# Performance work log

Hardware: AMD Instinct MI355X
Metric: run time of the kernel (lower is better)

## Reference

```python
import jax, jax.numpy as jnp
import numpy as np

B, C, H, W = 8, 512, 64, 64
NH, D = 8, 64            # num_heads, head_dim (C = NH*D)
WH, WW = 8, 8            # window size
EPS = 1e-5
SCALE = D ** -0.5


def _layernorm(x, g, b):
    mu = jnp.mean(x, axis=-1, keepdims=True)
    var = jnp.mean((x - mu) ** 2, axis=-1, keepdims=True)
    return (x - mu) * jax.lax.rsqrt(var + EPS) * g + b


def _rope_cache(n, d):
    pos = jnp.arange(n, dtype=jnp.float32)
    inv_freq = 1.0 / (10000.0 ** (jnp.arange(0, d, 2, dtype=jnp.float32) / d))
    sinusoid = pos[:, None] * inv_freq[None, :]          # (n, d//2)
    return jnp.stack([jnp.sin(sinusoid), jnp.cos(sinusoid)], axis=-1).reshape(n, d)


def _apply_rope(x, rope):
    # x: (B, nH, N, d); rope: (N, d) packed [sin, cos] interleaved
    b, nh, n, d = x.shape
    x_ = x.reshape(b, nh, n, d // 2, 2)
    r = rope.reshape(n, d // 2, 2)
    sin, cos = r[..., 0], r[..., 1]                      # (N, d//2)
    x0, x1 = x_[..., 0], x_[..., 1]
    xr0 = x0 * cos - x1 * sin
    xr1 = x0 * sin + x1 * cos
    return jnp.stack([xr0, xr1], axis=-1).reshape(b, nh, n, d)


def _relative_index(wh, ww):
    ch, cw = np.meshgrid(np.arange(wh), np.arange(ww), indexing='ij')
    flat = np.stack([ch.reshape(-1), cw.reshape(-1)])    # (2, Ws)
    rel = flat[:, :, None] - flat[:, None, :]            # (2, Ws, Ws)
    rel = rel.transpose(1, 2, 0).astype(np.int64)
    rel[..., 0] += wh - 1
    rel[..., 1] += ww - 1
    rel[..., 0] *= 2 * ww - 1
    return jnp.asarray(rel.sum(-1))                      # (Ws, Ws)


def setup_inputs() -> dict:
    key = jax.random.key(0)
    ks = jax.random.split(key, 12)
    s = 0.02
    table_size = (2 * WH - 1) * (2 * WW - 1)
    return {
        'q':  jax.random.normal(ks[0], (B, C, H, W), jnp.float32),
        'kv': jax.random.normal(ks[1], (B, C, H, W), jnp.float32),
        'g_q':  jnp.ones((C,), jnp.float32),  'b_q_ln':  jnp.zeros((C,), jnp.float32),
        'g_kv': jnp.ones((C,), jnp.float32),  'b_kv_ln': jnp.zeros((C,), jnp.float32),
        'Wq': jax.random.normal(ks[2], (C, C), jnp.float32) * s, 'bq': jnp.zeros((C,), jnp.float32),
        'Wk': jax.random.normal(ks[3], (C, C), jnp.float32) * s, 'bk': jnp.zeros((C,), jnp.float32),
        'Wv': jax.random.normal(ks[4], (C, C), jnp.float32) * s, 'bv': jnp.zeros((C,), jnp.float32),
        'Wo': jax.random.normal(ks[5], (C, C), jnp.float32) * s, 'bo': jnp.zeros((C,), jnp.float32),
        'bias_table': jax.random.normal(ks[6], (table_size, NH), jnp.float32) * s,
    }


def reference(q, kv, g_q, b_q_ln, g_kv, b_kv_ln, Wq, bq, Wk, bk, Wv, bv, Wo, bo, bias_table):
    N = H * W
    Hn, Wn = H // WH, W // WW
    nw = Hn * Wn
    Ws = WH * WW

    # flatten NCHW -> (B, N, C)
    q_seq = q.reshape(B, C, N).transpose(0, 2, 1)
    kv_seq = kv.reshape(B, C, N).transpose(0, 2, 1)
    q_seq = _layernorm(q_seq, g_q, b_q_ln)
    kv_seq = _layernorm(kv_seq, g_kv, b_kv_ln)

    Q = (q_seq @ Wq.T + bq).reshape(B, N, NH, D).transpose(0, 2, 1, 3)   # (B,nH,N,d)
    K = (kv_seq @ Wk.T + bk).reshape(B, N, NH, D).transpose(0, 2, 1, 3)
    V = (kv_seq @ Wv.T + bv).reshape(B, N, NH, D).transpose(0, 2, 1, 3)

    rope = _rope_cache(N, D)
    Q = _apply_rope(Q, rope)
    K = _apply_rope(K, rope)

    # window partition: (B,nH,H,W,d) -> (nH, B*nw, Ws, d); head-major to match torch cat order
    def part(x):
        x = x.reshape(B, NH, Hn, WH, Wn, WW, D)
        return x.transpose(1, 0, 2, 4, 3, 5, 6).reshape(NH, B * nw, Ws, D)

    Qw, Kw, Vw = part(Q), part(K), part(V)

    attn = jnp.einsum('hnqd,hnkd->hnqk', Qw, Kw) * SCALE                 # (nH, B*nw, Ws, Ws)
    rel_idx = _relative_index(WH, WW)
    bias = bias_table[rel_idx.reshape(-1)].reshape(Ws, Ws, NH).transpose(2, 0, 1)  # (nH, Ws, Ws)
    attn = attn + bias[:, None, :, :]
    attn = jax.nn.softmax(attn, axis=-1)
    out_w = jnp.einsum('hnqk,hnkd->hnqd', attn, Vw)                      # (nH, B*nw, Ws, d)

    # window reverse + head concat -> (B, N, C)
    out = out_w.reshape(NH, B, Hn, Wn, WH, WW, D)
    out = out.transpose(1, 2, 4, 3, 5, 0, 6).reshape(B, N, NH * D)

    out = out @ Wo.T + bo
    out = out + q_seq                                                    # residual w/ normed q (as in source)
    return out.transpose(0, 2, 1).reshape(B, C, H, W)
```

## Files before the change

### kernel.cpp

```cpp
#include <hip/hip_runtime.h>


typedef unsigned short u16;
typedef __bf16 bf16x8 __attribute__((ext_vector_type(8)));
typedef float f32x4 __attribute__((ext_vector_type(4)));
typedef u16 u16x8 __attribute__((ext_vector_type(8)));
typedef u16 u16x4 __attribute__((ext_vector_type(4)));

__device__ __forceinline__ u16 f2bf(float f) {
    __bf16 h = (__bf16)f;
    return __builtin_bit_cast(u16, h);
}
__device__ __forceinline__ float bf2f(u16 u) {
    return (float)__builtin_bit_cast(__bf16, u);
}
__device__ __forceinline__ f32x4 mfma16(bf16x8 a, bf16x8 b, f32x4 c) {
    return __builtin_amdgcn_mfma_f32_16x16x32_bf16(a, b, c, 0, 0, 0);
}
__device__ __forceinline__ void gl_lds16(const u16* g, u16* l) {
    __builtin_amdgcn_global_load_lds((const __attribute__((address_space(1))) void*)g,
                                     (__attribute__((address_space(3))) void*)l, 16, 0, 0);
}
__device__ __forceinline__ int swapb(int n) {
    return (n & 0xE07) | ((n & 0x1C0) >> 3) | ((n & 0x038) << 3);
}

__global__ __launch_bounds__(256) void prep_kernel(
    const float* __restrict__ q, const float* __restrict__ kv,
    const float* __restrict__ g_q, const float* __restrict__ b_q,
    const float* __restrict__ g_kv, const float* __restrict__ b_kv,
    const float* __restrict__ Wq, const float* __restrict__ Wk,
    const float* __restrict__ Wv, const float* __restrict__ Wo,
    const float* __restrict__ btab,
    u16* __restrict__ qn, u16* __restrict__ kvn,
    u16* __restrict__ wq, u16* __restrict__ wk,
    u16* __restrict__ wv, u16* __restrict__ wo,
    float* __restrict__ rope, float* __restrict__ biasf)
{
    __shared__ u16 sX[512 * 36];
    __shared__ float sS[1024];
    __shared__ float sQm[1024];
    __shared__ float sMu[32], sInv[32];

    const int bidx = blockIdx.x;
    const int tid = threadIdx.x;

    if (bidx >= 2048) {
        int idx = (bidx - 2048) * 256 + tid;
        {
            int w = idx >> 18, e = idx & 262143;
            const float* src = (w == 0) ? Wq : (w == 1) ? Wk : (w == 2) ? Wv : Wo;
            u16* dst = (w == 0) ? wq : (w == 1) ? wk : (w == 2) ? wv : wo;
            dst[e] = f2bf(src[e]);
        }
        if (idx < 131072) {
            int n = idx >> 5, j = idx & 31;
            float inv = powf(10000.0f, -(float)j / 32.0f);
            float a = (float)n * inv;
            float s, c;
            sincosf(a, &s, &c);
            rope[n * 64 + 2 * j] = s;
            rope[n * 64 + 2 * j + 1] = c;
        }
        if (idx < 32768) {
            int qq = idx & 63, pp = (idx >> 6) & 63, h = idx >> 12;
            int r1 = pp >> 3, c1 = pp & 7, r2 = qq >> 3, c2 = qq & 7;
            int ri = (r1 - r2 + 7) * 15 + (c1 - c2 + 7);
            biasf[idx] = btab[ri * 8 + h];
        }
        return;
    }

    const float* x  = (bidx < 1024) ? q : kv;
    const float* g  = (bidx < 1024) ? g_q : g_kv;
    const float* be = (bidx < 1024) ? b_q : b_kv;
    u16* out = (bidx < 1024) ? qn : kvn;
    const int bid = bidx & 1023;

    const int b = bid >> 7, grp = bid & 127;
    const int nbase = grp << 5;
    const int t4 = tid & 7;
    const int cg = tid >> 3;

    const float* xp = x + ((size_t)b << 21) + nbase + (t4 << 2);
    float sm[4] = {0.f, 0.f, 0.f, 0.f}, sq2[4] = {0.f, 0.f, 0.f, 0.f};
#pragma unroll 4
    for (int it = 0; it < 16; it++) {
        int c = (it << 5) + cg;
        f32x4 v = *(const f32x4*)&xp[(size_t)c << 12];
        u16x4 h;
#pragma unroll
        for (int r = 0; r < 4; r++) {
            sm[r] += v[r];
            sq2[r] += v[r] * v[r];
            h[r] = f2bf(v[r]);
        }
        *(u16x4*)&sX[c * 36 + (t4 << 2)] = h;
    }
#pragma unroll
    for (int r = 0; r < 4; r++) {
        sS[tid * 4 + r] = sm[r];
        sQm[tid * 4 + r] = sq2[r];
    }
    __syncthreads();
    if (tid < 32) {
        int t4v = tid >> 2, r = tid & 3;
        float a = 0.f, q2 = 0.f;
#pragma unroll
        for (int c2 = 0; c2 < 32; c2++) {
            int i2 = ((c2 << 3) + t4v) * 4 + r;
            a += sS[i2];
            q2 += sQm[i2];
        }
        float mu = a * (1.f / 512.f);
        float var = q2 * (1.f / 512.f) - mu * mu;
        sMu[tid] = mu;
        sInv[tid] = rsqrtf(var + 1e-5f);
    }
    __syncthreads();

    const int t = tid >> 3;
    const int cs = (tid & 7) << 3;
    float mu = sMu[t], inv = sInv[t];
    int p = swapb(nbase + t);
    size_t orow = ((size_t)((b << 12) + p)) * 512;
#pragma unroll
    for (int it = 0; it < 8; it++) {
        int c0 = cs + (it << 6);
        f32x4 g0 = *(const f32x4*)&g[c0];
        f32x4 g1 = *(const f32x4*)&g[c0 + 4];
        f32x4 e0 = *(const f32x4*)&be[c0];
        f32x4 e1 = *(const f32x4*)&be[c0 + 4];
        u16x8 o;
#pragma unroll
        for (int k = 0; k < 8; k++) {
            float v = bf2f(sX[(c0 + k) * 36 + t]);
            float gg = (k < 4) ? g0[k] : g1[k - 4];
            float bb = (k < 4) ? e0[k] : e1[k - 4];
            o[k] = f2bf((v - mu) * inv * gg + bb);
        }
        *(u16x8*)&out[orow + c0] = o;
    }
}

#define SB() __builtin_amdgcn_sched_barrier(0)
#define BARRIER() do { SB(); __builtin_amdgcn_s_barrier(); SB(); } while (0)
#define VM4() asm volatile("s_waitcnt vmcnt(4)" ::: "memory")
#define VM0() asm volatile("s_waitcnt vmcnt(0)" ::: "memory")
#define STAGE_A(base, kt, kk) do { \
        const u16* _g = aSt + (kt) * 64 + (kk) * 32; \
        gl_lds16(_g, &smem[(base) + (kk) * 8192 + wid * 512]); \
        gl_lds16(_g + 65536, &smem[(base) + (kk) * 8192 + 4096 + wid * 512]); \
    } while (0)
#define STAGE_B(base, kt, kk) do { \
        const u16* _g = bSt + (kt) * 64 + (kk) * 32; \
        gl_lds16(_g, &smem[(base) + (kk) * 8192 + wid * 512]); \
        gl_lds16(_g + 65536, &smem[(base) + (kk) * 8192 + 4096 + wid * 512]); \
    } while (0)
#define LDA(base, kk, mh) do { \
        Af[0] = *(const bf16x8*)&smem[(base) + (kk) * 8192 + (mh) * 2048 + 0 * 512 + aOff]; \
        Af[1] = *(const bf16x8*)&smem[(base) + (kk) * 8192 + (mh) * 2048 + 1 * 512 + aOff]; \
        Af[2] = *(const bf16x8*)&smem[(base) + (kk) * 8192 + (mh) * 2048 + 2 * 512 + aOff]; \
        Af[3] = *(const bf16x8*)&smem[(base) + (kk) * 8192 + (mh) * 2048 + 3 * 512 + aOff]; \
    } while (0)
#define LDB(base, kk) do { \
        Bf[0] = *(const bf16x8*)&smem[(base) + (kk) * 8192 + 0 * 512 + bOff]; \
        Bf[1] = *(const bf16x8*)&smem[(base) + (kk) * 8192 + 1 * 512 + bOff]; \
        Bf[2] = *(const bf16x8*)&smem[(base) + (kk) * 8192 + 2 * 512 + bOff]; \
        Bf[3] = *(const bf16x8*)&smem[(base) + (kk) * 8192 + 3 * 512 + bOff]; \
    } while (0)
#define MMA(mh) do { \
        __builtin_amdgcn_s_setprio(1); \
        _Pragma("unroll") \
        for (int fi = 0; fi < 4; ++fi) \
            _Pragma("unroll") \
            for (int j = 0; j < 4; ++j) \
                acc[(mh) * 4 + fi][j] = mfma16(Af[fi], Bf[j], acc[(mh) * 4 + fi][j]); \
        __builtin_amdgcn_s_setprio(0); \
    } while (0)

#define MAIN_LOOP_8PHASE() \
    STAGE_A(AX, 0, 0); \
    STAGE_B(BX, 0, 0); \
    STAGE_A(AX, 0, 1); \
    STAGE_B(BX, 0, 1); \
    VM4(); \
    BARRIER(); \
    _Pragma("unroll") \
    for (int it = 0; it < 4; ++it) { \
        const bool last = (it == 3); \
        bf16x8 Af[4], Bf[4]; \
        LDA(AX, 0, 0); LDB(BX, 0); STAGE_A(AY, 2 * it + 1, 0); \
        BARRIER(); MMA(0); BARRIER(); \
        LDA(AX, 0, 1); STAGE_B(BY, 2 * it + 1, 0); \
        BARRIER(); MMA(1); VM4(); BARRIER(); \
        LDA(AX, 1, 0); LDB(BX, 1); STAGE_A(AY, 2 * it + 1, 1); \
        BARRIER(); MMA(0); BARRIER(); \
        LDA(AX, 1, 1); STAGE_B(BY, 2 * it + 1, 1); \
        BARRIER(); MMA(1); VM4(); BARRIER(); \
        LDA(AY, 0, 0); LDB(BY, 0); if (!last) STAGE_A(AX, 2 * it + 2, 0); \
        BARRIER(); MMA(0); BARRIER(); \
        LDA(AY, 0, 1); if (!last) STAGE_B(BX, 2 * it + 2, 0); \
        BARRIER(); MMA(1); \
        if (!last) { VM4(); } else { VM0(); } \
        BARRIER(); \
        LDA(AY, 1, 0); LDB(BY, 1); if (!last) STAGE_A(AX, 2 * it + 2, 1); \
        BARRIER(); MMA(0); BARRIER(); \
        LDA(AY, 1, 1); if (!last) STAGE_B(BX, 2 * it + 2, 1); \
        BARRIER(); MMA(1); if (!last) VM4(); BARRIER(); \
    }

__global__ __launch_bounds__(512, 2) void gemm_qkv(
    const u16* __restrict__ qn, const u16* __restrict__ kvn,
    const u16* __restrict__ wq, const u16* __restrict__ wk, const u16* __restrict__ wv,
    const float* __restrict__ bq, const float* __restrict__ bk, const float* __restrict__ bv,
    const float* __restrict__ rope,
    u16* __restrict__ Qr, u16* __restrict__ Kr, u16* __restrict__ VT)
{
    __shared__ __align__(16) u16 smem[65536];

    const int bid = blockIdx.x;
    const int swz = (bid & 7) * 96 + (bid >> 3);
    const int kind = swz >> 8;
    const int rem = swz & 255;
    const int n0 = (rem >> 7) << 8;
    const int m0 = (rem & 127) << 8;

    const u16* Asrc = (kind == 0) ? qn : kvn;
    const u16* W = (kind == 0) ? wq : (kind == 1) ? wk : wv;
    const float* bias = (kind == 0) ? bq : (kind == 1) ? bk : bv;

    const int tid = threadIdx.x;
    const int lane = tid & 63, wid = tid >> 6;
    const int ln = lane & 15, lq = lane >> 4;
    const int wr = wid >> 2, wc = wid & 3;

    const int rr = tid >> 2;
    const int cc = (tid & 3) ^ ((tid >> 3) & 3);
    const u16* aSt = Asrc + (size_t)(m0 + rr) * 512 + cc * 8;
    const u16* bSt = W + (size_t)(n0 + rr) * 512 + cc * 8;

    const int AX = 0, BX = 16384, AY = 32768, BY = 49152;
    const int swzc = lq ^ ((ln >> 1) & 3);
    const int aOff = wr * 4096 + ln * 32 + swzc * 8;
    const int bOff = wc * 2048 + ln * 32 + swzc * 8;

    f32x4 acc[8][4] = {};

    MAIN_LOOP_8PHASE();

    float bj[4];
#pragma unroll
    for (int j = 0; j < 4; ++j) bj[j] = bias[n0 + wc * 64 + j * 16 + ln];

    u16* sU = smem;

    if (kind < 2) {
        u16* Out = (kind == 0) ? Qr : Kr;
#pragma unroll
        for (int g = 0; g < 4; ++g) {
            __syncthreads();
            if (wr == (g >> 1)) {
                const int i0 = (g & 1) * 4;
#pragma unroll
                for (int di = 0; di < 4; ++di)
#pragma unroll
                    for (int j = 0; j < 4; ++j)
#pragma unroll
                        for (int r = 0; r < 4; ++r)
                            sU[(di * 16 + lq * 4 + r) * 264 + wc * 64 + j * 16 + ln] =
                                f2bf(acc[i0 + di][j][r] + bj[j]);
            }
            __syncthreads();
#pragma unroll
            for (int it = 0; it < 4; ++it) {
                int idx = it * 512 + tid;
                int row = idx >> 5;
                int cseg = (idx & 31) << 3;
                u16x8 v = *(const u16x8*)&sU[row * 264 + cseg];
                int t = m0 + g * 64 + row;
                int n = swapb(t & 4095);
                float f[8];
#pragma unroll
                for (int k = 0; k < 8; k++) f[k] = bf2f(v[k]);
                {
                    int d0 = cseg & 63;
                    const float* rp = &rope[n * 64 + d0];
                    f32x4 r0 = *(const f32x4*)rp;
                    f32x4 r1 = *(const f32x4*)(rp + 4);
#pragma unroll
                    for (int pp = 0; pp < 4; pp++) {
                        float sn = (pp < 2) ? r0[2 * pp] : r1[2 * (pp - 2)];
                        float cs2 = (pp < 2) ? r0[2 * pp + 1] : r1[2 * (pp - 2) + 1];
                        float x0 = f[2 * pp], x1 = f[2 * pp + 1];
                        f[2 * pp] = x0 * cs2 - x1 * sn;
                        f[2 * pp + 1] = x0 * sn + x1 * cs2;
                    }
                }
                u16x8 o;
#pragma unroll
                for (int k = 0; k < 8; k++) o[k] = f2bf(f[k]);
                *(u16x8*)&Out[(size_t)t * 512 + n0 + cseg] = o;
            }
        }
    } else {
        const int wq0 = m0 & 4095;
        const int bb = m0 >> 12;
#pragma unroll
        for (int g = 0; g < 4; ++g) {
            __syncthreads();
            if (wc == g) {
#pragma unroll
                for (int i = 0; i < 8; ++i)
#pragma unroll
                    for (int j = 0; j < 4; ++j) {
                        u16x4 pk;
#pragma unroll
                        for (int r = 0; r < 4; ++r) pk[r] = f2bf(acc[i][j][r] + bj[j]);
                        *(u16x4*)&sU[(j * 16 + ln) * 264 + wr * 128 + i * 16 + lq * 4] = pk;
                    }
            }
            __syncthreads();
#pragma unroll
            for (int it = 0; it < 4; ++it) {
                int idx = it * 512 + tid;
                int col = idx >> 5;
                int ch = (idx & 31) << 3;
                u16x8 v = *(const u16x8*)&sU[col * 264 + ch];
                int c = n0 + g * 64 + col;
                int hh = c >> 6, dd = c & 63;
                *(u16x8*)&VT[((size_t)((((bb << 3) + hh) << 6) + dd)) * 4096 + wq0 + ch] = v;
            }
        }
    }
}

__global__ __launch_bounds__(512, 2) void gemm_out(
    const u16* __restrict__ A, const u16* __restrict__ Bw,
    const float* __restrict__ bias, const u16* __restrict__ qn,
    float* __restrict__ Out)
{
    __shared__ __align__(16) u16 smem[65536];

    const int bid = blockIdx.x;
    const int swz = (bid & 7) * 32 + (bid >> 3);
    const int n0 = (swz >> 7) << 8;
    const int m0 = (swz & 127) << 8;

    const int tid = threadIdx.x;
    const int lane = tid & 63, wid = tid >> 6;
    const int ln = lane & 15, lq = lane >> 4;
    const int wr = wid >> 2, wc = wid & 3;

    const int rr = tid >> 2;
    const int cc = (tid & 3) ^ ((tid >> 3) & 3);
    const u16* aSt = A + (size_t)(m0 + rr) * 512 + cc * 8;
    const u16* bSt = Bw + (size_t)(n0 + rr) * 512 + cc * 8;

    const int AX = 0, BX = 16384, AY = 32768, BY = 49152;
    const int swzc = lq ^ ((ln >> 1) & 3);
    const int aOff = wr * 4096 + ln * 32 + swzc * 8;
    const int bOff = wc * 2048 + ln * 32 + swzc * 8;

    f32x4 acc[8][4] = {};

    MAIN_LOOP_8PHASE();

    float bj[4];
#pragma unroll
    for (int j = 0; j < 4; ++j) bj[j] = bias[n0 + wc * 64 + j * 16 + ln];

    u16* sR = smem;
#pragma unroll
    for (int g = 0; g < 4; ++g) {
        __syncthreads();
#pragma unroll
        for (int it = 0; it < 4; ++it) {
            int idx = it * 512 + tid;
            int row = idx >> 5, c8 = (idx & 31) << 3;
            *(u16x8*)&sR[row * 264 + c8] =
                *(const u16x8*)&qn[(size_t)(m0 + g * 64 + row) * 512 + n0 + c8];
        }
        __syncthreads();
        if (wr == (g >> 1)) {
            const int i0 = (g & 1) * 4;
#pragma unroll
            for (int di = 0; di < 4; ++di) {
                int t0 = m0 + g * 64 + di * 16 + lq * 4;
                int bb = t0 >> 12;
                int nb = swapb(t0 & 4095);
                int lr = di * 16 + lq * 4;
#pragma unroll
                for (int j = 0; j < 4; ++j) {
                    int c = wc * 64 + j * 16 + ln;
                    f32x4 v;
#pragma unroll
                    for (int r = 0; r < 4; ++r)
                        v[r] = acc[i0 + di][j][r] + bj[j] + bf2f(sR[(lr + r) * 264 + c]);
                    *(f32x4*)&Out[((size_t)((bb << 9) + n0 + c) << 12) + nb] = v;
                }
            }
        }
    }
}

#undef SB
#undef BARRIER
#undef VM4
#undef VM0
#undef STAGE_A
#undef STAGE_B
#undef LDA
#undef LDB
#undef MMA
#undef MAIN_LOOP_8PHASE

__global__ __launch_bounds__(256) void attn_kernel(
    const u16* __restrict__ Q, const u16* __restrict__ K, const u16* __restrict__ VT,
    const float* __restrict__ biasf, u16* __restrict__ Out)
{
    __shared__ u16 sQ[64 * 72];
    __shared__ u16 sK[64 * 72];
    __shared__ u16 sVT[64 * 72];
    __shared__ u16 sP[4][16 * 72];

    const int tid = threadIdx.x;
    const int h = blockIdx.x & 7;
    const int w = (blockIdx.x >> 3) & 63;
    const int b = blockIdx.x >> 9;
    const int lane = tid & 63, wave = tid >> 6;
    const int ln = lane & 15, lq = lane >> 4;

    const size_t qrow0 = (size_t)(b << 12) + w * 64;
    const size_t vrow0 = ((size_t)(((b << 3) + h) << 6)) * 4096 + w * 64;

#pragma unroll
    for (int ii = 0; ii < 2; ii++) {
        int idx = ii * 256 + tid;
        int row = idx >> 3, ch = (idx & 7) << 3;
        size_t ga = (qrow0 + row) * 512 + h * 64 + ch;
        *(u16x8*)&sQ[row * 72 + ch] = *(const u16x8*)&Q[ga];
        *(u16x8*)&sK[row * 72 + ch] = *(const u16x8*)&K[ga];
        *(u16x8*)&sVT[row * 72 + ch] = *(const u16x8*)&VT[vrow0 + (size_t)row * 4096 + ch];
    }
    __syncthreads();

    f32x4 s[4] = {};
#pragma unroll
    for (int ks = 0; ks < 2; ks++) {
        bf16x8 a = *(const bf16x8*)&sQ[(wave * 16 + ln) * 72 + ks * 32 + lq * 8];
#pragma unroll
        for (int j = 0; j < 4; j++) {
            bf16x8 bb = *(const bf16x8*)&sK[(j * 16 + ln) * 72 + ks * 32 + lq * 8];
            s[j] = mfma16(a, bb, s[j]);
        }
    }

    float sv[4][4];
#pragma unroll
    for (int r = 0; r < 4; r++) {
        const float* bp = &biasf[((h * 64 + wave * 16 + lq * 4 + r) << 6) + ln];
#pragma unroll
        for (int j = 0; j < 4; j++) sv[r][j] = s[j][r] * 0.125f + bp[j * 16];
    }
#pragma unroll
    for (int r = 0; r < 4; r++) {
        float m = fmaxf(fmaxf(sv[r][0], sv[r][1]), fmaxf(sv[r][2], sv[r][3]));
        m = fmaxf(m, __shfl_xor(m, 1));
        m = fmaxf(m, __shfl_xor(m, 2));
        m = fmaxf(m, __shfl_xor(m, 4));
        m = fmaxf(m, __shfl_xor(m, 8));
        float sum = 0.f;
#pragma unroll
        for (int j = 0; j < 4; j++) {
            sv[r][j] = __expf(sv[r][j] - m);
            sum += sv[r][j];
        }
        sum += __shfl_xor(sum, 1);
        sum += __shfl_xor(sum, 2);
        sum += __shfl_xor(sum, 4);
        sum += __shfl_xor(sum, 8);
        float rinv = 1.f / sum;
#pragma unroll
        for (int j = 0; j < 4; j++)
            sP[wave][(lq * 4 + r) * 72 + j * 16 + ln] = f2bf(sv[r][j] * rinv);
    }

    f32x4 o[4] = {};
#pragma unroll
    for (int ks = 0; ks < 2; ks++) {
        bf16x8 a = *(const bf16x8*)&sP[wave][ln * 72 + ks * 32 + lq * 8];
#pragma unroll
        for (int jd = 0; jd < 4; jd++) {
            bf16x8 bb = *(const bf16x8*)&sVT[(jd * 16 + ln) * 72 + ks * 32 + lq * 8];
            o[jd] = mfma16(a, bb, o[jd]);
        }
    }

#pragma unroll
    for (int r = 0; r < 4; r++)
#pragma unroll
        for (int jd = 0; jd < 4; jd++)
            sQ[(wave * 16 + lq * 4 + r) * 72 + jd * 16 + ln] = f2bf(o[jd][r]);
    __syncthreads();
#pragma unroll
    for (int ii = 0; ii < 2; ii++) {
        int idx = ii * 256 + tid;
        int row = idx >> 3, ch = (idx & 7) << 3;
        *(u16x8*)&Out[(qrow0 + row) * 512 + h * 64 + ch] = *(const u16x8*)&sQ[row * 72 + ch];
    }
}

extern "C" void kernel_launch(void* const* d_in, const int* in_sizes, int n_in,
                              void* d_out, int out_size, void* d_ws, size_t ws_size,
                              hipStream_t stream)
{
    const float* q    = (const float*)d_in[0];
    const float* kv   = (const float*)d_in[1];
    const float* g_q  = (const float*)d_in[2];
    const float* b_q  = (const float*)d_in[3];
    const float* g_kv = (const float*)d_in[4];
    const float* b_kv = (const float*)d_in[5];
    const float* Wq   = (const float*)d_in[6];
    const float* bq   = (const float*)d_in[7];
    const float* Wk   = (const float*)d_in[8];
    const float* bk   = (const float*)d_in[9];
    const float* Wv   = (const float*)d_in[10];
    const float* bv   = (const float*)d_in[11];
    const float* Wo   = (const float*)d_in[12];
    const float* bo   = (const float*)d_in[13];
    const float* btab = (const float*)d_in[14];

    char* ws = (char*)d_ws;
    u16* qn      = (u16*)(ws);
    u16* kvn     = (u16*)(ws + 33554432);
    u16* VT      = (u16*)(ws + 67108864);
    float* rope  = (float*)(ws + 100663296);
    float* biasf = (float*)(ws + 101711872);
    u16* wq      = (u16*)(ws + 101842944);
    u16* wk      = (u16*)(ws + 102367232);
    u16* wv      = (u16*)(ws + 102891520);
    u16* wo      = (u16*)(ws + 103415808);
    u16* aout    = kvn;
    u16* Qr      = (u16*)d_out;
    u16* Kr      = Qr + 16777216;

    prep_kernel<<<6144, 256, 0, stream>>>(q, kv, g_q, b_q, g_kv, b_kv,
                                          Wq, Wk, Wv, Wo, btab,
                                          qn, kvn, wq, wk, wv, wo, rope, biasf);
    gemm_qkv<<<768, 512, 0, stream>>>(qn, kvn, wq, wk, wv, bq, bk, bv, rope, Qr, Kr, VT);
    attn_kernel<<<4096, 256, 0, stream>>>(Qr, Kr, VT, biasf, aout);
    gemm_out<<<256, 512, 0, stream>>>(aout, wo, bo, qn, (float*)d_out);
}
```

Baseline: 344.2 us.

## Stage gemm_out epilogue through LDS for coalesced NCHW stores; two heads per attention block

Result: slower. 380.5 us (+10.5%).

```diff
diff --git a/kernel.cpp b/kernel.cpp
--- a/kernel.cpp
+++ b/kernel.cpp
@@ -370,36 +370,46 @@
 #pragma unroll
     for (int j = 0; j < 4; ++j) bj[j] = bias[n0 + wc * 64 + j * 16 + ln];
 
-    u16* sR = smem;
-#pragma unroll
-    for (int g = 0; g < 4; ++g) {
+    float* sOutF = (float*)smem;
+    u16* sRes = smem + 33280;
+    const int bb = m0 >> 12;
+    const int swb = swapb(m0 & 4095);
+    const size_t outBase = ((size_t)((bb << 9) + n0)) << 12;
+
+#pragma unroll
+    for (int cg = 0; cg < 4; ++cg) {
         __syncthreads();
 #pragma unroll
-        for (int it = 0; it < 4; ++it) {
-            int idx = it * 512 + tid;
-            int row = idx >> 5, c8 = (idx & 31) << 3;
-            *(u16x8*)&sR[row * 264 + c8] =
-                *(const u16x8*)&qn[(size_t)(m0 + g * 64 + row) * 512 + n0 + c8];
+        for (int itq = 0; itq < 4; ++itq) {
+            int idx = itq * 512 + tid;
+            int row = idx >> 3, c8 = (idx & 7) << 3;
+            *(u16x8*)&sRes[row * 72 + c8] =
+                *(const u16x8*)&qn[(size_t)(m0 + row) * 512 + n0 + cg * 64 + c8];
         }
         __syncthreads();
-        if (wr == (g >> 1)) {
-            const int i0 = (g & 1) * 4;
-#pragma unroll
-            for (int di = 0; di < 4; ++di) {
-                int t0 = m0 + g * 64 + di * 16 + lq * 4;
-                int bb = t0 >> 12;
-                int nb = swapb(t0 & 4095);
-                int lr = di * 16 + lq * 4;
-#pragma unroll
-                for (int j = 0; j < 4; ++j) {
-                    int c = wc * 64 + j * 16 + ln;
-                    f32x4 v;
-#pragma unroll
-                    for (int r = 0; r < 4; ++r)
-                        v[r] = acc[i0 + di][j][r] + bj[j] + bf2f(sR[(lr + r) * 264 + c]);
-                    *(f32x4*)&Out[((size_t)((bb << 9) + n0 + c) << 12) + nb] = v;
-                }
-            }
+        if (wc == cg) {
+#pragma unroll
+            for (int i = 0; i < 8; ++i)
+#pragma unroll
+                for (int j = 0; j < 4; ++j)
+#pragma unroll
+                    for (int r = 0; r < 4; ++r) {
+                        int row = wr * 128 + i * 16 + lq * 4 + r;
+                        int c = j * 16 + ln;
+                        sOutF[row * 65 + c] =
+                            acc[i][j][r] + bj[j] + bf2f(sRes[row * 72 + c]);
+                    }
+        }
+        __syncthreads();
+#pragma unroll
+        for (int li = 0; li < 8; ++li) {
+            int u = li * 512 + tid;
+            int c = u >> 6, r3 = (u >> 3) & 7, op = u & 7;
+            int base_i = ((op & 1) << 2) + (r3 << 3) + ((op >> 1) << 6);
+            f32x4 v;
+#pragma unroll
+            for (int r = 0; r < 4; ++r) v[r] = sOutF[(base_i + r) * 65 + c];
+            *(f32x4*)&Out[outBase + ((size_t)(cg * 64 + c) << 12) + swb + r3 * 64 + op * 4] = v;
         }
     }
 }
@@ -415,43 +425,18 @@
 #undef MMA
 #undef MAIN_LOOP_8PHASE
 
-__global__ __launch_bounds__(256) void attn_kernel(
-    const u16* __restrict__ Q, const u16* __restrict__ K, const u16* __restrict__ VT,
-    const float* __restrict__ biasf, u16* __restrict__ Out)
+__device__ __forceinline__ void attn_tile(
+    const u16* __restrict__ sQp, const u16* __restrict__ sKp,
+    const u16* __restrict__ sVTp, u16* __restrict__ sPp,
+    const float* __restrict__ biasf, int h, int wave, int ln, int lq, f32x4 o[4])
 {
-    __shared__ u16 sQ[64 * 72];
-    __shared__ u16 sK[64 * 72];
-    __shared__ u16 sVT[64 * 72];
-    __shared__ u16 sP[4][16 * 72];
-
-    const int tid = threadIdx.x;
-    const int h = blockIdx.x & 7;
-    const int w = (blockIdx.x >> 3) & 63;
-    const int b = blockIdx.x >> 9;
-    const int lane = tid & 63, wave = tid >> 6;
-    const int ln = lane & 15, lq = lane >> 4;
-
-    const size_t qrow0 = (size_t)(b << 12) + w * 64;
-    const size_t vrow0 = ((size_t)(((b << 3) + h) << 6)) * 4096 + w * 64;
-
-#pragma unroll
-    for (int ii = 0; ii < 2; ii++) {
-        int idx = ii * 256 + tid;
-        int row = idx >> 3, ch = (idx & 7) << 3;
-        size_t ga = (qrow0 + row) * 512 + h * 64 + ch;
-        *(u16x8*)&sQ[row * 72 + ch] = *(const u16x8*)&Q[ga];
-        *(u16x8*)&sK[row * 72 + ch] = *(const u16x8*)&K[ga];
-        *(u16x8*)&sVT[row * 72 + ch] = *(const u16x8*)&VT[vrow0 + (size_t)row * 4096 + ch];
-    }
-    __syncthreads();
-
     f32x4 s[4] = {};
 #pragma unroll
     for (int ks = 0; ks < 2; ks++) {
-        bf16x8 a = *(const bf16x8*)&sQ[(wave * 16 + ln) * 72 + ks * 32 + lq * 8];
+        bf16x8 a = *(const bf16x8*)&sQp[(wave * 16 + ln) * 72 + ks * 32 + lq * 8];
 #pragma unroll
         for (int j = 0; j < 4; j++) {
-            bf16x8 bb = *(const bf16x8*)&sK[(j * 16 + ln) * 72 + ks * 32 + lq * 8];
+            bf16x8 bb = *(const bf16x8*)&sKp[(j * 16 + ln) * 72 + ks * 32 + lq * 8];
             s[j] = mfma16(a, bb, s[j]);
         }
     }
@@ -483,31 +468,105 @@
         float rinv = 1.f / sum;
 #pragma unroll
         for (int j = 0; j < 4; j++)
-            sP[wave][(lq * 4 + r) * 72 + j * 16 + ln] = f2bf(sv[r][j] * rinv);
-    }
-
-    f32x4 o[4] = {};
+            sPp[(lq * 4 + r) * 72 + j * 16 + ln] = f2bf(sv[r][j] * rinv);
+    }
+
+    o[0] = f32x4{0.f, 0.f, 0.f, 0.f};
+    o[1] = f32x4{0.f, 0.f, 0.f, 0.f};
+    o[2] = f32x4{0.f, 0.f, 0.f, 0.f};
+    o[3] = f32x4{0.f, 0.f, 0.f, 0.f};
 #pragma unroll
     for (int ks = 0; ks < 2; ks++) {
-        bf16x8 a = *(const bf16x8*)&sP[wave][ln * 72 + ks * 32 + lq * 8];
+        bf16x8 a = *(const bf16x8*)&sPp[ln * 72 + ks * 32 + lq * 8];
 #pragma unroll
         for (int jd = 0; jd < 4; jd++) {
-            bf16x8 bb = *(const bf16x8*)&sVT[(jd * 16 + ln) * 72 + ks * 32 + lq * 8];
+            bf16x8 bb = *(const bf16x8*)&sVTp[(jd * 16 + ln) * 72 + ks * 32 + lq * 8];
             o[jd] = mfma16(a, bb, o[jd]);
         }
     }
-
-#pragma unroll
-    for (int r = 0; r < 4; r++)
-#pragma unroll
-        for (int jd = 0; jd < 4; jd++)
-            sQ[(wave * 16 + lq * 4 + r) * 72 + jd * 16 + ln] = f2bf(o[jd][r]);
-    __syncthreads();
+}
+
+__global__ __launch_bounds__(256) void attn_kernel(
+    const u16* __restrict__ Q, const u16* __restrict__ K, const u16* __restrict__ VT,
+    const float* __restrict__ biasf, u16* __restrict__ Out)
+{
+    __shared__ u16 sQ[2][64 * 72];
+    __shared__ u16 sK[2][64 * 72];
+    __shared__ u16 sVT[2][64 * 72];
+    __shared__ u16 sP[2][4][16 * 72];
+
+    const int tid = threadIdx.x;
+    const int code0 = blockIdx.x << 1;
+    const int h0 = code0 & 7;
+    const int w = (code0 >> 3) & 63;
+    const int b = code0 >> 9;
+    const int lane = tid & 63, wave = tid >> 6;
+    const int ln = lane & 15, lq = lane >> 4;
+
+    const size_t qrow0 = (size_t)(b << 12) + w * 64;
+
+    u16x8 rq[2][2], rk[2][2], rv[2][2];
+#pragma unroll
+    for (int t = 0; t < 2; ++t) {
+        const int h = h0 + t;
+        const size_t vrow0 = ((size_t)(((b << 3) + h) << 6)) * 4096 + w * 64;
+#pragma unroll
+        for (int ii = 0; ii < 2; ii++) {
+            int idx = ii * 256 + tid;
+            int rw = idx >> 3, ch = (idx & 7) << 3;
+            size_t ga = (qrow0 + rw) * 512 + h * 64 + ch;
+            rq[t][ii] = *(const u16x8*)&Q[ga];
+            rk[t][ii] = *(const u16x8*)&K[ga];
+            rv[t][ii] = *(const u16x8*)&VT[vrow0 + (size_t)rw * 4096 + ch];
+        }
+    }
 #pragma unroll
     for (int ii = 0; ii < 2; ii++) {
         int idx = ii * 256 + tid;
-        int row = idx >> 3, ch = (idx & 7) << 3;
-        *(u16x8*)&Out[(qrow0 + row) * 512 + h * 64 + ch] = *(const u16x8*)&sQ[row * 72 + ch];
+        int rw = idx >> 3, ch = (idx & 7) << 3;
+        *(u16x8*)&sQ[0][rw * 72 + ch] = rq[0][ii];
+        *(u16x8*)&sK[0][rw * 72 + ch] = rk[0][ii];
+        *(u16x8*)&sVT[0][rw * 72 + ch] = rv[0][ii];
+    }
+    __syncthreads();
+
+    f32x4 o[4];
+    attn_tile(sQ[0], sK[0], sVT[0], sP[0][wave], biasf, h0, wave, ln, lq, o);
+
+#pragma unroll
+    for (int ii = 0; ii < 2; ii++) {
+        int idx = ii * 256 + tid;
+        int rw = idx >> 3, ch = (idx & 7) << 3;
+        *(u16x8*)&sQ[1][rw * 72 + ch] = rq[1][ii];
+        *(u16x8*)&sK[1][rw * 72 + ch] = rk[1][ii];
+        *(u16x8*)&sVT[1][rw * 72 + ch] = rv[1][ii];
+    }
+#pragma unroll
+    for (int r = 0; r < 4; r++)
+#pragma unroll
+        for (int jd = 0; jd < 4; jd++)
+            sQ[0][(wave * 16 + lq * 4 + r) * 72 + jd * 16 + ln] = f2bf(o[jd][r]);
+    __syncthreads();
+
+#pragma unroll
+    for (int ii = 0; ii < 2; ii++) {
+        int idx = ii * 256 + tid;
+        int rw = idx >> 3, ch = (idx & 7) << 3;
+        *(u16x8*)&Out[(qrow0 + rw) * 512 + h0 * 64 + ch] = *(const u16x8*)&sQ[0][rw * 72 + ch];
+    }
+    attn_tile(sQ[1], sK[1], sVT[1], sP[1][wave], biasf, h0 + 1, wave, ln, lq, o);
+#pragma unroll
+    for (int r = 0; r < 4; r++)
+#pragma unroll
+        for (int jd = 0; jd < 4; jd++)
+            sQ[1][(wave * 16 + lq * 4 + r) * 72 + jd * 16 + ln] = f2bf(o[jd][r]);
+    __syncthreads();
+#pragma unroll
+    for (int ii = 0; ii < 2; ii++) {
+        int idx = ii * 256 + tid;
+        int rw = idx >> 3, ch = (idx & 7) << 3;
+        *(u16x8*)&Out[(qrow0 + rw) * 512 + (h0 + 1) * 64 + ch] =
+            *(const u16x8*)&sQ[1][rw * 72 + ch];
     }
 }
 
@@ -549,6 +608,6 @@
                                           Wq, Wk, Wv, Wo, btab,
                                           qn, kvn, wq, wk, wv, wo, rope, biasf);
     gemm_qkv<<<768, 512, 0, stream>>>(qn, kvn, wq, wk, wv, bq, bk, bv, rope, Qr, Kr, VT);
-    attn_kernel<<<4096, 256, 0, stream>>>(Qr, Kr, VT, biasf, aout);
+    attn_kernel<<<2048, 256, 0, stream>>>(Qr, Kr, VT, biasf, aout);
     gemm_out<<<256, 512, 0, stream>>>(aout, wo, bo, qn, (float*)d_out);
 }
```

## Make QKV GEMM persistent with cross-tile prefetch and restructure output epilogues

Applied to the files above, without the earlier changes.

After: 344.6 us. About the same (+0.1%).

```diff
diff --git a/kernel.cpp b/kernel.cpp
--- a/kernel.cpp
+++ b/kernel.cpp
@@ -4,6 +4,7 @@
 typedef unsigned short u16;
 typedef __bf16 bf16x8 __attribute__((ext_vector_type(8)));
 typedef float f32x4 __attribute__((ext_vector_type(4)));
+typedef float f32x2 __attribute__((ext_vector_type(2)));
 typedef u16 u16x8 __attribute__((ext_vector_type(8)));
 typedef u16 u16x4 __attribute__((ext_vector_type(4)));
 
@@ -46,23 +47,29 @@
     const int tid = threadIdx.x;
 
     if (bidx >= 2048) {
-        int idx = (bidx - 2048) * 256 + tid;
-        {
-            int w = idx >> 18, e = idx & 262143;
+        if (bidx < 3072) {
+            int idx = (bidx - 2048) * 256 + tid;
+            int w = idx >> 16, qd = idx & 65535;
             const float* src = (w == 0) ? Wq : (w == 1) ? Wk : (w == 2) ? Wv : Wo;
             u16* dst = (w == 0) ? wq : (w == 1) ? wk : (w == 2) ? wv : wo;
-            dst[e] = f2bf(src[e]);
-        }
-        if (idx < 131072) {
+            f32x4 v = *(const f32x4*)&src[qd * 4];
+            u16x4 h;
+#pragma unroll
+            for (int r = 0; r < 4; r++) h[r] = f2bf(v[r]);
+            *(u16x4*)&dst[qd * 4] = h;
+        } else if (bidx < 3584) {
+            int idx = (bidx - 3072) * 256 + tid;
             int n = idx >> 5, j = idx & 31;
             float inv = powf(10000.0f, -(float)j / 32.0f);
             float a = (float)n * inv;
             float s, c;
             sincosf(a, &s, &c);
-            rope[n * 64 + 2 * j] = s;
-            rope[n * 64 + 2 * j + 1] = c;
-        }
-        if (idx < 32768) {
+            f32x2 sc;
+            sc[0] = s;
+            sc[1] = c;
+            *(f32x2*)&rope[n * 64 + 2 * j] = sc;
+        } else {
+            int idx = (bidx - 3584) * 256 + tid;
             int qq = idx & 63, pp = (idx >> 6) & 63, h = idx >> 12;
             int r1 = pp >> 3, c1 = pp & 7, r2 = qq >> 3, c2 = qq & 7;
             int ri = (r1 - r2 + 7) * 15 + (c1 - c2 + 7);
@@ -84,7 +91,7 @@
 
     const float* xp = x + ((size_t)b << 21) + nbase + (t4 << 2);
     float sm[4] = {0.f, 0.f, 0.f, 0.f}, sq2[4] = {0.f, 0.f, 0.f, 0.f};
-#pragma unroll 4
+#pragma unroll 8
     for (int it = 0; it < 16; it++) {
         int c = (it << 5) + cg;
         f32x4 v = *(const f32x4*)&xp[(size_t)c << 12];
@@ -147,15 +154,17 @@
 #define BARRIER() do { SB(); __builtin_amdgcn_s_barrier(); SB(); } while (0)
 #define VM4() asm volatile("s_waitcnt vmcnt(4)" ::: "memory")
 #define VM0() asm volatile("s_waitcnt vmcnt(0)" ::: "memory")
-#define STAGE_A(base, kt, kk) do { \
-        const u16* _g = aSt + (kt) * 64 + (kk) * 32; \
+#define VM20() asm volatile("s_waitcnt vmcnt(20)" ::: "memory")
+#define STAGE_P(ptr, base, kt, kk) do { \
+        const u16* _g = (ptr) + (kt) * 64 + (kk) * 32; \
         gl_lds16(_g, &smem[(base) + (kk) * 8192 + wid * 512]); \
         gl_lds16(_g + 65536, &smem[(base) + (kk) * 8192 + 4096 + wid * 512]); \
     } while (0)
-#define STAGE_B(base, kt, kk) do { \
-        const u16* _g = bSt + (kt) * 64 + (kk) * 32; \
-        gl_lds16(_g, &smem[(base) + (kk) * 8192 + wid * 512]); \
-        gl_lds16(_g + 65536, &smem[(base) + (kk) * 8192 + 4096 + wid * 512]); \
+#define PROLOGUE4(aP, bP) do { \
+        STAGE_P(aP, AX, 0, 0); \
+        STAGE_P(bP, BX, 0, 0); \
+        STAGE_P(aP, AX, 0, 1); \
+        STAGE_P(bP, BX, 0, 1); \
     } while (0)
 #define LDA(base, kk, mh) do { \
         Af[0] = *(const bf16x8*)&smem[(base) + (kk) * 8192 + (mh) * 2048 + 0 * 512 + aOff]; \
@@ -179,34 +188,32 @@
         __builtin_amdgcn_s_setprio(0); \
     } while (0)
 
-#define MAIN_LOOP_8PHASE() \
-    STAGE_A(AX, 0, 0); \
-    STAGE_B(BX, 0, 0); \
-    STAGE_A(AX, 0, 1); \
-    STAGE_B(BX, 0, 1); \
-    VM4(); \
+#define MAIN_LOOP_8PHASE(WARM) \
+    if (WARM) { VM20(); } else { VM4(); } \
     BARRIER(); \
     _Pragma("unroll") \
     for (int it = 0; it < 4; ++it) { \
         const bool last = (it == 3); \
         bf16x8 Af[4], Bf[4]; \
-        LDA(AX, 0, 0); LDB(BX, 0); STAGE_A(AY, 2 * it + 1, 0); \
+        LDA(AX, 0, 0); LDB(BX, 0); STAGE_P(aSt, AY, 2 * it + 1, 0); \
         BARRIER(); MMA(0); BARRIER(); \
-        LDA(AX, 0, 1); STAGE_B(BY, 2 * it + 1, 0); \
+        LDA(AX, 0, 1); STAGE_P(bSt, BY, 2 * it + 1, 0); \
+        BARRIER(); MMA(1); \
+        if ((WARM) && it == 0) { VM20(); } else { VM4(); } \
+        BARRIER(); \
+        LDA(AX, 1, 0); LDB(BX, 1); STAGE_P(aSt, AY, 2 * it + 1, 1); \
+        BARRIER(); MMA(0); BARRIER(); \
+        LDA(AX, 1, 1); STAGE_P(bSt, BY, 2 * it + 1, 1); \
         BARRIER(); MMA(1); VM4(); BARRIER(); \
-        LDA(AX, 1, 0); LDB(BX, 1); STAGE_A(AY, 2 * it + 1, 1); \
+        LDA(AY, 0, 0); LDB(BY, 0); if (!last) STAGE_P(aSt, AX, 2 * it + 2, 0); \
         BARRIER(); MMA(0); BARRIER(); \
-        LDA(AX, 1, 1); STAGE_B(BY, 2 * it + 1, 1); \
-        BARRIER(); MMA(1); VM4(); BARRIER(); \
-        LDA(AY, 0, 0); LDB(BY, 0); if (!last) STAGE_A(AX, 2 * it + 2, 0); \
-        BARRIER(); MMA(0); BARRIER(); \
-        LDA(AY, 0, 1); if (!last) STAGE_B(BX, 2 * it + 2, 0); \
+        LDA(AY, 0, 1); if (!last) STAGE_P(bSt, BX, 2 * it + 2, 0); \
         BARRIER(); MMA(1); \
         if (!last) { VM4(); } else { VM0(); } \
         BARRIER(); \
-        LDA(AY, 1, 0); LDB(BY, 1); if (!last) STAGE_A(AX, 2 * it + 2, 1); \
+        LDA(AY, 1, 0); LDB(BY, 1); if (!last) STAGE_P(aSt, AX, 2 * it + 2, 1); \
         BARRIER(); MMA(0); BARRIER(); \
-        LDA(AY, 1, 1); if (!last) STAGE_B(BX, 2 * it + 2, 1); \
+        LDA(AY, 1, 1); if (!last) STAGE_P(bSt, BX, 2 * it + 2, 1); \
         BARRIER(); MMA(1); if (!last) VM4(); BARRIER(); \
     }
 
@@ -219,17 +226,7 @@
 {
     __shared__ __align__(16) u16 smem[65536];
 
-    const int bid = blockIdx.x;
-    const int swz = (bid & 7) * 96 + (bid >> 3);
-    const int kind = swz >> 8;
-    const int rem = swz & 255;
-    const int n0 = (rem >> 7) << 8;
-    const int m0 = (rem & 127) << 8;
-
-    const u16* Asrc = (kind == 0) ? qn : kvn;
-    const u16* W = (kind == 0) ? wq : (kind == 1) ? wk : wv;
-    const float* bias = (kind == 0) ? bq : (kind == 1) ? bk : bv;
-
+    const int p = blockIdx.x;
     const int tid = threadIdx.x;
     const int lane = tid & 63, wid = tid >> 6;
     const int ln = lane & 15, lq = lane >> 4;
@@ -237,102 +234,138 @@
 
     const int rr = tid >> 2;
     const int cc = (tid & 3) ^ ((tid >> 3) & 3);
-    const u16* aSt = Asrc + (size_t)(m0 + rr) * 512 + cc * 8;
-    const u16* bSt = W + (size_t)(n0 + rr) * 512 + cc * 8;
 
     const int AX = 0, BX = 16384, AY = 32768, BY = 49152;
     const int swzc = lq ^ ((ln >> 1) & 3);
     const int aOff = wr * 4096 + ln * 32 + swzc * 8;
     const int bOff = wc * 2048 + ln * 32 + swzc * 8;
 
-    f32x4 acc[8][4] = {};
-
-    MAIN_LOOP_8PHASE();
-
-    float bj[4];
-#pragma unroll
-    for (int j = 0; j < 4; ++j) bj[j] = bias[n0 + wc * 64 + j * 16 + ln];
-
-    u16* sU = smem;
-
-    if (kind < 2) {
-        u16* Out = (kind == 0) ? Qr : Kr;
-#pragma unroll
-        for (int g = 0; g < 4; ++g) {
-            __syncthreads();
-            if (wr == (g >> 1)) {
-                const int i0 = (g & 1) * 4;
-#pragma unroll
-                for (int di = 0; di < 4; ++di)
-#pragma unroll
-                    for (int j = 0; j < 4; ++j)
-#pragma unroll
-                        for (int r = 0; r < 4; ++r)
-                            sU[(di * 16 + lq * 4 + r) * 264 + wc * 64 + j * 16 + ln] =
-                                f2bf(acc[i0 + di][j][r] + bj[j]);
+    const u16* aSt;
+    const u16* bSt;
+    const float* bias;
+    int kind, n0, m0;
+
+#define DECODE(VID) do { \
+        int _swz = ((VID) & 7) * 96 + ((VID) >> 3); \
+        kind = _swz >> 8; \
+        int _rem = _swz & 255; \
+        n0 = (_rem >> 7) << 8; \
+        m0 = (_rem & 127) << 8; \
+        const u16* _As = (kind == 0) ? qn : kvn; \
+        const u16* _W = (kind == 0) ? wq : (kind == 1) ? wk : wv; \
+        bias = (kind == 0) ? bq : (kind == 1) ? bk : bv; \
+        aSt = _As + (size_t)(m0 + rr) * 512 + cc * 8; \
+        bSt = _W + (size_t)(n0 + rr) * 512 + cc * 8; \
+    } while (0)
+
+    f32x4 acc[8][4];
+
+    DECODE(p);
+    PROLOGUE4(aSt, bSt);
+
+#pragma unroll 1
+    for (int item = 0; item < 3; ++item) {
+#pragma unroll
+        for (int i = 0; i < 8; ++i)
+#pragma unroll
+            for (int j = 0; j < 4; ++j) acc[i][j] = f32x4{0.f, 0.f, 0.f, 0.f};
+
+        const bool warm = (item != 0);
+        MAIN_LOOP_8PHASE(warm);
+
+        const int ek = kind, en0 = n0, em0 = m0;
+        const float* ebias = bias;
+        if (item < 2) {
+            DECODE((item + 1) * 256 + p);
+            PROLOGUE4(aSt, bSt);
+        }
+
+        float bj[4];
+#pragma unroll
+        for (int j = 0; j < 4; ++j) bj[j] = ebias[en0 + wc * 64 + j * 16 + ln];
+
+        u16* sU = smem + 32768;
+
+        if (ek < 2) {
+            u16* Out = (ek == 0) ? Qr : Kr;
+#pragma unroll
+            for (int g = 0; g < 4; ++g) {
+                __syncthreads();
+                if (wr == (g >> 1)) {
+                    const int i0 = (g & 1) * 4;
+#pragma unroll
+                    for (int di = 0; di < 4; ++di)
+#pragma unroll
+                        for (int j = 0; j < 4; ++j)
+#pragma unroll
+                            for (int r = 0; r < 4; ++r)
+                                sU[(di * 16 + lq * 4 + r) * 264 + wc * 64 + j * 16 + ln] =
+                                    f2bf(acc[i0 + di][j][r] + bj[j]);
+                }
+                __syncthreads();
+#pragma unroll
+                for (int it = 0; it < 4; ++it) {
+                    int idx = it * 512 + tid;
+                    int row = idx >> 5;
+                    int cseg = (idx & 31) << 3;
+                    u16x8 v = *(const u16x8*)&sU[row * 264 + cseg];
+                    int t = em0 + g * 64 + row;
+                    int n = swapb(t & 4095);
+                    float f[8];
+#pragma unroll
+                    for (int k = 0; k < 8; k++) f[k] = bf2f(v[k]);
+                    {
+                        int d0 = cseg & 63;
+                        const float* rp = &rope[n * 64 + d0];
+                        f32x4 r0 = *(const f32x4*)rp;
+                        f32x4 r1 = *(const f32x4*)(rp + 4);
+#pragma unroll
+                        for (int pp = 0; pp < 4; pp++) {
+                            float sn = (pp < 2) ? r0[2 * pp] : r1[2 * (pp - 2)];
+                            float cs2 = (pp < 2) ? r0[2 * pp + 1] : r1[2 * (pp - 2) + 1];
+                            float x0 = f[2 * pp], x1 = f[2 * pp + 1];
+                            f[2 * pp] = x0 * cs2 - x1 * sn;
+                            f[2 * pp + 1] = x0 * sn + x1 * cs2;
+                        }
+                    }
+                    u16x8 o;
+#pragma unroll
+                    for (int k = 0; k < 8; k++) o[k] = f2bf(f[k]);
+                    *(u16x8*)&Out[(size_t)t * 512 + en0 + cseg] = o;
+                }
             }
-            __syncthreads();
-#pragma unroll
-            for (int it = 0; it < 4; ++it) {
-                int idx = it * 512 + tid;
-                int row = idx >> 5;
-                int cseg = (idx & 31) << 3;
-                u16x8 v = *(const u16x8*)&sU[row * 264 + cseg];
-                int t = m0 + g * 64 + row;
-                int n = swapb(t & 4095);
-                float f[8];
-#pragma unroll
-                for (int k = 0; k < 8; k++) f[k] = bf2f(v[k]);
-                {
-                    int d0 = cseg & 63;
-                    const float* rp = &rope[n * 64 + d0];
-                    f32x4 r0 = *(const f32x4*)rp;
-                    f32x4 r1 = *(const f32x4*)(rp + 4);
-#pragma unroll
-                    for (int pp = 0; pp < 4; pp++) {
-                        float sn = (pp < 2) ? r0[2 * pp] : r1[2 * (pp - 2)];
-                        float cs2 = (pp < 2) ? r0[2 * pp + 1] : r1[2 * (pp - 2) + 1];
-                        float x0 = f[2 * pp], x1 = f[2 * pp + 1];
-                        f[2 * pp] = x0 * cs2 - x1 * sn;
-                        f[2 * pp + 1] = x0 * sn + x1 * cs2;
-                    }
+        } else {
+            const int wq0 = em0 & 4095;
+            const int bb = em0 >> 12;
+#pragma unroll
+            for (int g = 0; g < 4; ++g) {
+                __syncthreads();
+                if (wc == g) {
+#pragma unroll
+                    for (int i = 0; i < 8; ++i)
+#pragma unroll
+                        for (int j = 0; j < 4; ++j) {
+                            u16x4 pk;
+#pragma unroll
+                            for (int r = 0; r < 4; ++r) pk[r] = f2bf(acc[i][j][r] + bj[j]);
+                            *(u16x4*)&sU[(j * 16 + ln) * 264 + wr * 128 + i * 16 + lq * 4] = pk;
+                        }
                 }
-                u16x8 o;
-#pragma unroll
-                for (int k = 0; k < 8; k++) o[k] = f2bf(f[k]);
-                *(u16x8*)&Out[(size_t)t * 512 + n0 + cseg] = o;
+                __syncthreads();
+#pragma unroll
+                for (int it = 0; it < 4; ++it) {
+                    int idx = it * 512 + tid;
+                    int col = idx >> 5;
+                    int ch = (idx & 31) << 3;
+                    u16x8 v = *(const u16x8*)&sU[col * 264 + ch];
+                    int c = en0 + g * 64 + col;
+                    int hh = c >> 6, dd = c & 63;
+                    *(u16x8*)&VT[((size_t)((((bb << 3) + hh) << 6) + dd)) * 4096 + wq0 + ch] = v;
+                }
             }
         }
-    } else {
-        const int wq0 = m0 & 4095;
-        const int bb = m0 >> 12;
-#pragma unroll
-        for (int g = 0; g < 4; ++g) {
-            __syncthreads();
-            if (wc == g) {
-#pragma unroll
-                for (int i = 0; i < 8; ++i)
-#pragma unroll
-                    for (int j = 0; j < 4; ++j) {
-                        u16x4 pk;
-#pragma unroll
-                        for (int r = 0; r < 4; ++r) pk[r] = f2bf(acc[i][j][r] + bj[j]);
-                        *(u16x4*)&sU[(j * 16 + ln) * 264 + wr * 128 + i * 16 + lq * 4] = pk;
-                    }
-            }
-            __syncthreads();
-#pragma unroll
-            for (int it = 0; it < 4; ++it) {
-                int idx = it * 512 + tid;
-                int col = idx >> 5;
-                int ch = (idx & 31) << 3;
-                u16x8 v = *(const u16x8*)&sU[col * 264 + ch];
-                int c = n0 + g * 64 + col;
-                int hh = c >> 6, dd = c & 63;
-                *(u16x8*)&VT[((size_t)((((bb << 3) + hh) << 6) + dd)) * 4096 + wq0 + ch] = v;
-            }
-        }
-    }
+    }
+#undef DECODE
 }
 
 __global__ __launch_bounds__(512, 2) void gemm_out(
@@ -364,42 +397,53 @@
 
     f32x4 acc[8][4] = {};
 
-    MAIN_LOOP_8PHASE();
+    PROLOGUE4(aSt, bSt);
+    MAIN_LOOP_8PHASE(false);
 
     float bj[4];
 #pragma unroll
     for (int j = 0; j < 4; ++j) bj[j] = bias[n0 + wc * 64 + j * 16 + ln];
 
-    u16* sR = smem;
-#pragma unroll
-    for (int g = 0; g < 4; ++g) {
+    float* sOutF = (float*)smem;
+    u16* sRes = smem + 33280;
+    const int bb = m0 >> 12;
+    const int swb = swapb(m0 & 4095);
+    const size_t outBase = ((size_t)((bb << 9) + n0)) << 12;
+
+#pragma unroll
+    for (int cg = 0; cg < 4; ++cg) {
         __syncthreads();
 #pragma unroll
-        for (int it = 0; it < 4; ++it) {
-            int idx = it * 512 + tid;
-            int row = idx >> 5, c8 = (idx & 31) << 3;
-            *(u16x8*)&sR[row * 264 + c8] =
-                *(const u16x8*)&qn[(size_t)(m0 + g * 64 + row) * 512 + n0 + c8];
+        for (int itq = 0; itq < 4; ++itq) {
+            int idx = itq * 512 + tid;
+            int row = idx >> 3, c8 = (idx & 7) << 3;
+            *(u16x8*)&sRes[row * 72 + c8] =
+                *(const u16x8*)&qn[(size_t)(m0 + row) * 512 + n0 + cg * 64 + c8];
         }
         __syncthreads();
-        if (wr == (g >> 1)) {
-            const int i0 = (g & 1) * 4;
-#pragma unroll
-            for (int di = 0; di < 4; ++di) {
-                int t0 = m0 + g * 64 + di * 16 + lq * 4;
-                int bb = t0 >> 12;
-                int nb = swapb(t0 & 4095);
-                int lr = di * 16 + lq * 4;
-#pragma unroll
-                for (int j = 0; j < 4; ++j) {
-                    int c = wc * 64 + j * 16 + ln;
-                    f32x4 v;
-#pragma unroll
-                    for (int r = 0; r < 4; ++r)
-                        v[r] = acc[i0 + di][j][r] + bj[j] + bf2f(sR[(lr + r) * 264 + c]);
-                    *(f32x4*)&Out[((size_t)((bb << 9) + n0 + c) << 12) + nb] = v;
-                }
-            }
+        if (wc == cg) {
+#pragma unroll
+            for (int i = 0; i < 8; ++i)
+#pragma unroll
+                for (int j = 0; j < 4; ++j)
+#pragma unroll
+                    for (int r = 0; r < 4; ++r) {
+                        int row = wr * 128 + i * 16 + lq * 4 + r;
+                        int c = j * 16 + ln;
+                        sOutF[row * 65 + c] =
+                            acc[i][j][r] + bj[j] + bf2f(sRes[row * 72 + c]);
+                    }
+        }
+        __syncthreads();
+#pragma unroll
+        for (int li = 0; li < 8; ++li) {
+            int u = li * 512 + tid;
+            int c = u >> 6, r3 = (u >> 3) & 7, op = u & 7;
+            int base_i = ((op & 1) << 2) + (r3 << 3) + ((op >> 1) << 6);
+            f32x4 v;
+#pragma unroll
+            for (int r = 0; r < 4; ++r) v[r] = sOutF[(base_i + r) * 65 + c];
+            *(f32x4*)&Out[outBase + ((size_t)(cg * 64 + c) << 12) + swb + r3 * 64 + op * 4] = v;
         }
     }
 }
@@ -408,8 +452,9 @@
 #undef BARRIER
 #undef VM4
 #undef VM0
-#undef STAGE_A
-#undef STAGE_B
+#undef VM20
+#undef STAGE_P
+#undef PROLOGUE4
 #undef LDA
 #undef LDB
 #undef MMA
@@ -545,10 +590,10 @@
     u16* Qr      = (u16*)d_out;
     u16* Kr      = Qr + 16777216;
 
-    prep_kernel<<<6144, 256, 0, stream>>>(q, kv, g_q, b_q, g_kv, b_kv,
+    prep_kernel<<<3712, 256, 0, stream>>>(q, kv, g_q, b_q, g_kv, b_kv,
                                           Wq, Wk, Wv, Wo, btab,
                                           qn, kvn, wq, wk, wv, wo, rope, biasf);
-    gemm_qkv<<<768, 512, 0, stream>>>(qn, kvn, wq, wk, wv, bq, bk, bv, rope, Qr, Kr, VT);
+    gemm_qkv<<<256, 512, 0, stream>>>(qn, kvn, wq, wk, wv, bq, bk, bv, rope, Qr, Kr, VT);
     attn_kernel<<<4096, 256, 0, stream>>>(Qr, Kr, VT, biasf, aout);
     gemm_out<<<256, 512, 0, stream>>>(aout, wo, bo, qn, (float*)d_out);
 }
```
